# Performance work log

Measured on AMD Instinct MI355X. Metric: run time of the kernel, lower is better.

Reference implementation:

```python
import jax, jax.numpy as jnp
import numpy as np

B, S, L, U, E, V = 32, 64, 64, 512, 256, 32000

def setup_inputs() -> dict:
    key = jax.random.key(0)
    ks = jax.random.split(key, 12)
    sc = lambda *d: 0.02
    return {
        "target": jax.random.randint(ks[0], (B, S), 0, V),
        "encoder_outputs": jax.random.normal(ks[1], (B, L, U), jnp.float32),
        "enc_h0": jax.random.normal(ks[2], (B, U), jnp.float32),
        "enc_c0": jax.random.normal(ks[3], (B, U), jnp.float32),
        "emb": jax.random.normal(ks[4], (V, E), jnp.float32) * 0.02,
        "W_x": jax.random.normal(ks[5], (E, 4 * U), jnp.float32) * 0.02,
        "W_h": jax.random.normal(ks[6], (U, 4 * U), jnp.float32) * 0.02,
        "b_lstm": jnp.zeros((4 * U,), jnp.float32),
        "Wa": jax.random.normal(ks[7], (U, U), jnp.float32) * 0.02,
        "W_fc": jax.random.normal(ks[8], (2 * U, V), jnp.float32) * 0.02,
        "b_fc": jnp.zeros((V,), jnp.float32),
    }

def reference(target, encoder_outputs, enc_h0, enc_c0, emb, W_x, W_h, b_lstm, Wa, W_fc, b_fc):
    # Teacher forcing (teach_forcing_ran=1): input at step t is target[:, t-1],
    # producing outputs for t = 1 .. seq_maxlen-1.
    x_seq = emb[target[:, : S - 1]]                      # [B, S-1, E]
    x_seq = jnp.transpose(x_seq, (1, 0, 2))              # [S-1, B, E]
    enc_proj = jnp.einsum('blu,uv->blv', encoder_outputs, Wa)  # Luong 'general' projection

    def step(carry, x_t):
        h, c = carry
        z = x_t @ W_x + h @ W_h + b_lstm                 # [B, 4U]
        i, f, g, o = jnp.split(z, 4, axis=-1)            # keras gate order i,f,c,o
        i = jax.nn.sigmoid(i); f = jax.nn.sigmoid(f)
        g = jnp.tanh(g);       o = jax.nn.sigmoid(o)
        c = f * c + i * g
        h = o * jnp.tanh(c)
        score = jnp.einsum('bu,blu->bl', h, enc_proj)    # [B, L]
        attn = jax.nn.softmax(score, axis=-1)
        ctx = jnp.einsum('bl,blu->bu', attn, encoder_outputs)
        logits = jnp.tanh(jnp.concatenate([ctx, h], axis=-1) @ W_fc + b_fc)
        out_t = jax.nn.log_softmax(logits, axis=-1)      # [B, V]
        return (h, c), out_t

    (_, _), outs = jax.lax.scan(step, (enc_h0, enc_c0), x_seq)
    return jnp.transpose(outs, (1, 0, 2))                # [B, S-1, V]
```

## Files before the change

### kernel.cpp

```cpp
#include <hip/hip_runtime.h>
#include <stdint.h>

#define B_   32
#define T_   63
#define U_   512
#define E_   256
#define V_   32000
#define L_   64
#define FU_  2048
#define KFC_ 1024
#define MROW_ 2016

#define NFCX_ 250
#define NFCY_ 16
#define CCNT_BASE 1024

typedef float f32x4 __attribute__((ext_vector_type(4)));
typedef float f32x2 __attribute__((ext_vector_type(2)));
typedef __bf16 bf16x8 __attribute__((ext_vector_type(8)));

__device__ __forceinline__ unsigned short f2bf(float f) {
  union { float f; unsigned u; } v; v.f = f;
  unsigned u = v.u;
  u += 0x7FFFu + ((u >> 16) & 1u);
  return (unsigned short)(u >> 16);
}
__device__ __forceinline__ float bf2f(unsigned short h) {
  union { unsigned u; float f; } v; v.u = ((unsigned)h) << 16;
  return v.f;
}
__device__ __forceinline__ float fast_sigmoid(float x) {
  return 1.f / (1.f + __expf(-x));
}
__device__ __forceinline__ float fast_tanh(float x) {
  float e = __expf(2.f * x);
  return 1.f - 2.f / (e + 1.f);
}

__global__ __launch_bounds__(256) void k_prep(const int* __restrict__ target,
    const float* __restrict__ emb, const float* __restrict__ W_x,
    const float* __restrict__ b_lstm, const float* __restrict__ enc_out,
    const float* __restrict__ Wa, const float* __restrict__ W_h,
    const float* __restrict__ W_fc,
    unsigned short* __restrict__ fragWh, unsigned short* __restrict__ Zx,
    float* __restrict__ enc_proj, unsigned short* __restrict__ encT,
    unsigned short* __restrict__ WfcT,
    unsigned int* __restrict__ hcnt, float* __restrict__ row_sums) {
  __shared__ __align__(16) char smem[32768];
  const int bx = blockIdx.x;
  const int tid = threadIdx.x;

  if (bx < 512) {
    int idx = bx * 256 + tid;
    int lane = idx & 63;
    int kc   = (idx >> 6) & 15;
    int ct   = idx >> 10;
    int quad = lane >> 4, l15 = lane & 15;
    int col = ct * 16 + l15;
    unsigned short* dst = fragWh + (size_t)idx * 8;
#pragma unroll
    for (int j = 0; j < 8; ++j) {
      int k = kc * 32 + quad * 8 + j;
      dst[j] = f2bf(W_h[(size_t)k * FU_ + col]);
    }
  } else if (bx < 1016) {
    float* x_lds = (float*)smem;
    int r = bx - 512;
    int t = r % 63, cc = r / 63;
    for (int i = tid; i < B_ * E_; i += 256) {
      int b = i >> 8, e = i & 255;
      x_lds[i] = emb[(size_t)target[b * 64 + t] * E_ + e];
    }
    __syncthreads();
    int col = cc * 256 + tid;
    float acc[B_];
#pragma unroll
    for (int b = 0; b < B_; ++b) acc[b] = 0.f;
    for (int e4 = 0; e4 < E_ / 4; ++e4) {
      float w0 = W_x[(size_t)(4 * e4 + 0) * FU_ + col];
      float w1 = W_x[(size_t)(4 * e4 + 1) * FU_ + col];
      float w2 = W_x[(size_t)(4 * e4 + 2) * FU_ + col];
      float w3 = W_x[(size_t)(4 * e4 + 3) * FU_ + col];
#pragma unroll
      for (int b = 0; b < B_; ++b) {
        f32x4 xv = *(const f32x4*)&x_lds[b * E_ + 4 * e4];
        acc[b] += xv[0] * w0 + xv[1] * w1 + xv[2] * w2 + xv[3] * w3;
      }
    }
    float bias = b_lstm[col];
#pragma unroll
    for (int b = 0; b < B_; ++b)
      Zx[((size_t)(t * B_ + b)) * FU_ + col] = f2bf(acc[b] + bias);
  } else if (bx < 1272) {
    float* e_lds = (float*)smem;
    int r = bx - 1016;
    int rc = r & 127, cc = r >> 7;
    int row0 = rc * 16;
    for (int i = tid; i < 16 * U_; i += 256)
      e_lds[i] = enc_out[(size_t)(row0 + (i >> 9)) * U_ + (i & 511)];
    __syncthreads();
    int col = cc * 256 + tid;
    float acc[16];
#pragma unroll
    for (int q = 0; q < 16; ++q) acc[q] = 0.f;
    for (int k4 = 0; k4 < U_ / 4; ++k4) {
      float w0 = Wa[(size_t)(4 * k4 + 0) * U_ + col];
      float w1 = Wa[(size_t)(4 * k4 + 1) * U_ + col];
      float w2 = Wa[(size_t)(4 * k4 + 2) * U_ + col];
      float w3 = Wa[(size_t)(4 * k4 + 3) * U_ + col];
#pragma unroll
      for (int q = 0; q < 16; ++q) {
        f32x4 xv = *(const f32x4*)&e_lds[q * U_ + 4 * k4];
        acc[q] += xv[0] * w0 + xv[1] * w1 + xv[2] * w2 + xv[3] * w3;
      }
    }
#pragma unroll
    for (int q = 0; q < 16; ++q)
      enc_proj[(size_t)(row0 + q) * U_ + col] = acc[q];
  } else if (bx < 1528) {
    float (*tile)[65] = (float(*)[65])smem;
    int r = bx - 1272;
    int b = r & 31, uc = r >> 5;
#pragma unroll
    for (int i = 0; i < 16; ++i) {
      int idx = i * 256 + tid;
      int l = idx >> 6, u = idx & 63;
      tile[l][u] = enc_out[((size_t)b * L_ + l) * U_ + uc * 64 + u];
    }
    __syncthreads();
#pragma unroll
    for (int i = 0; i < 16; ++i) {
      int idx = i * 256 + tid;
      int u = idx >> 6, l = idx & 63;
      encT[((size_t)b * U_ + uc * 64 + u) * L_ + l] = f2bf(tile[l][u]);
    }
  } else if (bx < 1536) {
    int i = (bx - 1528) * 256 + tid;
    if (i < 2048) hcnt[i] = 0u;
    if (i < MROW_) row_sums[i] = 0.f;
  } else {
    float (*tile)[33] = (float(*)[33])smem;
    int r = bx - 1536;
    int nb = r % 1000, kb = r / 1000;
    int rr = tid >> 5, c = tid & 31;
#pragma unroll
    for (int i = 0; i < 4; ++i)
      tile[rr + 8 * i][c] = W_fc[(size_t)(kb * 32 + rr + 8 * i) * V_ + nb * 32 + c];
    __syncthreads();
#pragma unroll
    for (int i = 0; i < 4; ++i)
      WfcT[(size_t)(nb * 32 + rr + 8 * i) * KFC_ + kb * 32 + c] = f2bf(tile[c][rr + 8 * i]);
  }
}

__global__ __launch_bounds__(256, 1) void k_rec(const float* __restrict__ enc_h0,
    const float* __restrict__ enc_c0,
    const float* __restrict__ enc_proj, const unsigned short* __restrict__ Zx,
    const unsigned short* __restrict__ fragWh, const unsigned short* __restrict__ encT,
    unsigned int* hseq32,
    unsigned short* __restrict__ Afc,
    unsigned int* hcnt,
    const unsigned short* __restrict__ WfcT, const float* __restrict__ b_fc,
    float* __restrict__ out, float* __restrict__ row_sums) {
  __shared__ __align__(16) char smem[44160];

  const int tid = threadIdx.x;
  unsigned long long* hseq64 = (unsigned long long*)hseq32;

  if (blockIdx.x < 32) {
    unsigned short* h_lds = (unsigned short*)smem;
    float* z_lds = (float*)(smem + 33280);
    float* c_lds = (float*)(smem + 41984);

    const int g = blockIdx.x;
    const int w = tid >> 6;
    const int lane = tid & 63;
    const int quad = lane >> 4;
    const int l15 = lane & 15;
    const int b = tid >> 3;
    const int j = tid & 7;

    const unsigned short* bbase = fragWh + ((size_t)(w * 32 + g) * 16) * 64 * 8;
    bf16x8 bfr[16];
#pragma unroll
    for (int kc = 0; kc < 16; ++kc)
      bfr[kc] = *(const bf16x8*)(bbase + (size_t)(kc * 64 + lane) * 8);

    {
      int u = g * 16 + 2 * j;
      float h0a = enc_h0[(size_t)b * U_ + u];
      float h0b = enc_h0[(size_t)b * U_ + u + 1];
      unsigned pack = (unsigned)f2bf(h0a) | ((unsigned)f2bf(h0b) << 16);
      __hip_atomic_store(&hseq32[b * 256 + g * 8 + j], pack,
                         __ATOMIC_RELAXED, __HIP_MEMORY_SCOPE_AGENT);
      c_lds[b * 17 + 2 * j]     = enc_c0[(size_t)b * U_ + u];
      c_lds[b * 17 + 2 * j + 1] = enc_c0[(size_t)b * U_ + u + 1];
    }
    __syncthreads();
    if (tid == 0)
      __hip_atomic_fetch_add(&hcnt[0], 1u, __ATOMIC_RELAXED, __HIP_MEMORY_SCOPE_AGENT);

    for (int t = 0; t < T_; ++t) {
      const unsigned short* zxbase = Zx + ((size_t)(t * B_ + b)) * FU_ + g * 16 + 2 * j;
      unsigned zxp0 = *(const unsigned*)(zxbase + 0 * U_);
      unsigned zxp1 = *(const unsigned*)(zxbase + 1 * U_);
      unsigned zxp2 = *(const unsigned*)(zxbase + 2 * U_);
      unsigned zxp3 = *(const unsigned*)(zxbase + 3 * U_);

      if (tid == 0) {
        while (__hip_atomic_load(&hcnt[t * 16], __ATOMIC_RELAXED,
                                 __HIP_MEMORY_SCOPE_AGENT) < 32u)
          __builtin_amdgcn_s_sleep(1);
      }
      __syncthreads();

      const unsigned long long* hp = hseq64 + (size_t)t * (B_ * U_ / 4);
#pragma unroll
      for (int i = 0; i < 16; ++i) {
        int idx = i * 256 + tid;
        int hb = idx >> 7, u0 = (idx & 127) * 4;
        unsigned long long v = __hip_atomic_load(&hp[idx], __ATOMIC_RELAXED,
                                                 __HIP_MEMORY_SCOPE_AGENT);
        *(unsigned long long*)&h_lds[hb * 520 + u0] = v;
      }
      __syncthreads();

      f32x4 acc0 = {0.f, 0.f, 0.f, 0.f}, acc1 = {0.f, 0.f, 0.f, 0.f};
#pragma unroll
      for (int kc = 0; kc < 16; ++kc) {
        bf16x8 a0 = *(const bf16x8*)&h_lds[l15 * 520 + kc * 32 + quad * 8];
        bf16x8 a1 = *(const bf16x8*)&h_lds[(16 + l15) * 520 + kc * 32 + quad * 8];
        acc0 = __builtin_amdgcn_mfma_f32_16x16x32_bf16(a0, bfr[kc], acc0, 0, 0, 0);
        acc1 = __builtin_amdgcn_mfma_f32_16x16x32_bf16(a1, bfr[kc], acc1, 0, 0, 0);
      }
#pragma unroll
      for (int r = 0; r < 4; ++r) {
        z_lds[(quad * 4 + r) * 68 + w * 16 + l15] = acc0[r];
        z_lds[(16 + quad * 4 + r) * 68 + w * 16 + l15] = acc1[r];
      }
      __syncthreads();

      {
        int up0 = 2 * j, up1 = 2 * j + 1;
        float zi0 = z_lds[b * 68 + 0 + up0] + bf2f((unsigned short)(zxp0 & 0xFFFFu));
        float zi1 = z_lds[b * 68 + 0 + up1] + bf2f((unsigned short)(zxp0 >> 16));
        float zf0 = z_lds[b * 68 + 16 + up0] + bf2f((unsigned short)(zxp1 & 0xFFFFu));
        float zf1 = z_lds[b * 68 + 16 + up1] + bf2f((unsigned short)(zxp1 >> 16));
        float zg0 = z_lds[b * 68 + 32 + up0] + bf2f((unsigned short)(zxp2 & 0xFFFFu));
        float zg1 = z_lds[b * 68 + 32 + up1] + bf2f((unsigned short)(zxp2 >> 16));
        float zo0 = z_lds[b * 68 + 48 + up0] + bf2f((unsigned short)(zxp3 & 0xFFFFu));
        float zo1 = z_lds[b * 68 + 48 + up1] + bf2f((unsigned short)(zxp3 >> 16));
        float i0 = fast_sigmoid(zi0), i1 = fast_sigmoid(zi1);
        float f0 = fast_sigmoid(zf0), f1 = fast_sigmoid(zf1);
        float g0 = fast_tanh(zg0),    g1 = fast_tanh(zg1);
        float o0 = fast_sigmoid(zo0), o1 = fast_sigmoid(zo1);
        float c0 = f0 * c_lds[b * 17 + up0] + i0 * g0;
        float c1 = f1 * c_lds[b * 17 + up1] + i1 * g1;
        c_lds[b * 17 + up0] = c0;
        c_lds[b * 17 + up1] = c1;
        float h0 = o0 * fast_tanh(c0);
        float h1 = o1 * fast_tanh(c1);
        unsigned pack = (unsigned)f2bf(h0) | ((unsigned)f2bf(h1) << 16);
        __hip_atomic_store(&hseq32[(size_t)(t + 1) * (B_ * U_ / 2) + b * 256 + g * 8 + j],
                           pack, __ATOMIC_RELAXED, __HIP_MEMORY_SCOPE_AGENT);
        __hip_atomic_store(
            (unsigned*)&Afc[(size_t)(t * B_ + b) * KFC_ + U_ + g * 16 + 2 * j],
            pack, __ATOMIC_RELAXED, __HIP_MEMORY_SCOPE_AGENT);
      }
      __syncthreads();
      if (tid == 0)
        __hip_atomic_fetch_add(&hcnt[(t + 1) * 16], 1u,
                               __ATOMIC_RELAXED, __HIP_MEMORY_SCOPE_AGENT);
    }
  } else if (blockIdx.x < 64) {
    float* h_sh    = (float*)smem;
    float* sc_part = (float*)(smem + 2048);
    float* probs   = (float*)(smem + 3072);

    const int b = blockIdx.x - 32;
    for (int t = 0; t < T_; ++t) {
      if (tid == 0) {
        while (__hip_atomic_load(&hcnt[(t + 1) * 16], __ATOMIC_RELAXED,
                                 __HIP_MEMORY_SCOPE_AGENT) < 32u)
          __builtin_amdgcn_s_sleep(2);
      }
      __syncthreads();
      if (tid < 128) {
        unsigned long long v = __hip_atomic_load(
            &hseq64[(size_t)(t + 1) * (B_ * U_ / 4) + b * 128 + tid],
            __ATOMIC_RELAXED, __HIP_MEMORY_SCOPE_AGENT);
        int u0 = tid * 4;
        h_sh[u0 + 0] = bf2f((unsigned short)(v & 0xFFFFu));
        h_sh[u0 + 1] = bf2f((unsigned short)((v >> 16) & 0xFFFFu));
        h_sh[u0 + 2] = bf2f((unsigned short)((v >> 32) & 0xFFFFu));
        h_sh[u0 + 3] = bf2f((unsigned short)((v >> 48) & 0xFFFFu));
      }
      __syncthreads();
      {
        int l = tid & 63, part = tid >> 6;
        const float* ep = enc_proj + ((size_t)(b * L_ + l)) * U_ + part * 128;
        const float* hs = h_sh + part * 128;
        float s = 0.f;
#pragma unroll 8
        for (int u = 0; u < 128; u += 4) {
          f32x4 e = *(const f32x4*)(ep + u);
          s += hs[u] * e[0] + hs[u + 1] * e[1] + hs[u + 2] * e[2] + hs[u + 3] * e[3];
        }
        sc_part[part * L_ + l] = s;
      }
      __syncthreads();
      if (tid < 64) {
        float s = sc_part[tid] + sc_part[64 + tid] + sc_part[128 + tid] + sc_part[192 + tid];
        float m = s;
#pragma unroll
        for (int off = 32; off >= 1; off >>= 1) m = fmaxf(m, __shfl_xor(m, off));
        float e = __expf(s - m);
        float sum = e;
#pragma unroll
        for (int off = 32; off >= 1; off >>= 1) sum += __shfl_xor(sum, off);
        probs[tid] = e / sum;
      }
      __syncthreads();
      {
        int u0 = 2 * tid;
        const unsigned short* ep0 = encT + ((size_t)b * U_ + u0) * L_;
        float c0 = 0.f, c1 = 0.f;
#pragma unroll
        for (int l8 = 0; l8 < 8; ++l8) {
          bf16x8 e0 = *(const bf16x8*)(ep0 + l8 * 8);
          bf16x8 e1 = *(const bf16x8*)(ep0 + L_ + l8 * 8);
#pragma unroll
          for (int q = 0; q < 8; ++q) {
            float p = probs[l8 * 8 + q];
            c0 += p * (float)e0[q];
            c1 += p * (float)e1[q];
          }
        }
        unsigned pack = (unsigned)f2bf(c0) | ((unsigned)f2bf(c1) << 16);
        __hip_atomic_store((unsigned*)&Afc[(size_t)(t * B_ + b) * KFC_ + u0], pack,
                           __ATOMIC_RELAXED, __HIP_MEMORY_SCOPE_AGENT);
      }
      __syncthreads();
      if (tid == 0)
        __hip_atomic_fetch_add(&hcnt[CCNT_BASE + t * 16], 1u,
                               __ATOMIC_RELAXED, __HIP_MEMORY_SCOPE_AGENT);
    }
  } else {
    unsigned short* At = (unsigned short*)smem;
    unsigned short* Bt = (unsigned short*)(smem + 8192);
    float* rs = (float*)(smem + 16384);

    const int idx = blockIdx.x - 64;
    const int cx = idx % NFCX_, ry = idx / NFCX_;
    int t_hi = 4 * ry + 3; if (t_hi > T_ - 1) t_hi = T_ - 1;

    if (tid == 0) {
      while (__hip_atomic_load(&hcnt[CCNT_BASE + t_hi * 16], __ATOMIC_RELAXED,
                               __HIP_MEMORY_SCOPE_AGENT) < 32u)
        __builtin_amdgcn_s_sleep(32);
    }
    __syncthreads();

    const int w = tid >> 6, lane = tid & 63, quad = lane >> 4, l15 = lane & 15;
    const int row0 = ry * 128, col0 = cx * 128;
    const int mh = (w >> 1) * 64, nh = (w & 1) * 64;

    f32x4 acc[4][4];
#pragma unroll
    for (int i = 0; i < 4; ++i)
#pragma unroll
      for (int j = 0; j < 4; ++j) { f32x4 z = {0.f, 0.f, 0.f, 0.f}; acc[i][j] = z; }

    for (int kt = 0; kt < KFC_ / 32; ++kt) {
      int k0 = kt * 32;
#pragma unroll
      for (int i = 0; i < 2; ++i) {
        int lin = i * 256 + tid;
        int r = lin >> 2, s = lin & 3;
        int gseg = (s - (r >> 1)) & 3;
        f32x4 va = *(const f32x4*)(Afc + ((size_t)(row0 + r)) * KFC_ + k0 + gseg * 8);
        *(f32x4*)&At[r * 32 + s * 8] = va;
        f32x4 vb = *(const f32x4*)(WfcT + ((size_t)(col0 + r)) * KFC_ + k0 + gseg * 8);
        *(f32x4*)&Bt[r * 32 + s * 8] = vb;
      }
      __syncthreads();
      bf16x8 a[4], b[4];
#pragma unroll
      for (int i = 0; i < 4; ++i) {
        int m = mh + i * 16 + l15;
        a[i] = *(const bf16x8*)&At[m * 32 + (((quad + (m >> 1)) & 3) * 8)];
        int n = nh + i * 16 + l15;
        b[i] = *(const bf16x8*)&Bt[n * 32 + (((quad + (n >> 1)) & 3) * 8)];
      }
#pragma unroll
      for (int i = 0; i < 4; ++i)
#pragma unroll
        for (int j = 0; j < 4; ++j)
          acc[i][j] = __builtin_amdgcn_mfma_f32_16x16x32_bf16(a[i], b[j], acc[i][j], 0, 0, 0);
      __syncthreads();
    }

    if (tid < 128) rs[tid] = 0.f;
    __syncthreads();
    float bv[4];
#pragma unroll
    for (int j = 0; j < 4; ++j) bv[j] = b_fc[col0 + nh + j * 16 + l15];
    float rp[4][4];
#pragma unroll
    for (int i = 0; i < 4; ++i)
#pragma unroll
      for (int r = 0; r < 4; ++r) rp[i][r] = 0.f;
#pragma unroll
    for (int i = 0; i < 4; ++i) {
#pragma unroll
      for (int j = 0; j < 4; ++j) {
        int cg = col0 + nh + j * 16 + l15;
#pragma unroll
        for (int r = 0; r < 4; ++r) {
          float val = fast_tanh(acc[i][j][r] + bv[j]);
          int rg = row0 + mh + i * 16 + quad * 4 + r;
          if (rg < MROW_) {
            int b = rg & 31, t = rg >> 5;
            out[((size_t)(b * T_ + t)) * V_ + cg] = val;
          }
          rp[i][r] += __expf(val);
        }
      }
    }
#pragma unroll
    for (int i = 0; i < 4; ++i)
#pragma unroll
      for (int r = 0; r < 4; ++r) {
        float v = rp[i][r];
        v += __shfl_xor(v, 1); v += __shfl_xor(v, 2);
        v += __shfl_xor(v, 4); v += __shfl_xor(v, 8);
        if (l15 == 0) atomicAdd(&rs[mh + i * 16 + quad * 4 + r], v);
      }
    __syncthreads();
    if (tid < 128) {
      int rg = row0 + tid;
      if (rg < MROW_) atomicAdd(&row_sums[rg], rs[tid]);
    }
  }
}

__global__ __launch_bounds__(256) void k_lsm(float* __restrict__ out,
                                             const float* __restrict__ row_sums, int n4) {
  int i = blockIdx.x * 256 + threadIdx.x;
  if (i >= n4) return;
  f32x4* o4 = (f32x4*)out;
  f32x4 v = o4[i];
  int r = i / 8000;
  int b = r / 63, t = r - b * 63;
  float ls = __logf(row_sums[t * 32 + b]);
  v[0] -= ls; v[1] -= ls; v[2] -= ls; v[3] -= ls;
  o4[i] = v;
}

extern "C" void kernel_launch(void* const* d_in, const int* in_sizes, int n_in,
                              void* d_out, int out_size, void* d_ws, size_t ws_size,
                              hipStream_t stream) {
  const int*   target  = (const int*)d_in[0];
  const float* enc_out = (const float*)d_in[1];
  const float* enc_h0  = (const float*)d_in[2];
  const float* enc_c0  = (const float*)d_in[3];
  const float* emb     = (const float*)d_in[4];
  const float* W_x     = (const float*)d_in[5];
  const float* W_h     = (const float*)d_in[6];
  const float* b_lstm  = (const float*)d_in[7];
  const float* Wa      = (const float*)d_in[8];
  const float* W_fc    = (const float*)d_in[9];
  const float* b_fc    = (const float*)d_in[10];
  float* out = (float*)d_out;
  char* ws = (char*)d_ws;

  unsigned int*   hcnt     = (unsigned int*)(ws + 0);
  float*          row_sums = (float*)(ws + 8192);
  unsigned short* fragWh   = (unsigned short*)(ws + 16384);
  unsigned int*   hseq32   = (unsigned int*)(ws + 2113536);
  unsigned short* Zx       = (unsigned short*)(ws + 4210688);
  float*          enc_proj = (float*)(ws + 12468224);
  unsigned short* Afc      = (unsigned short*)(ws + 16662528);
  unsigned short* encT     = (unsigned short*)(ws + 20856832);
  unsigned short* WfcT     = (unsigned short*)(ws + 22953984);

  k_prep <<<dim3(33536),        dim3(256), 0, stream>>>(target, emb, W_x, b_lstm,
                                                        enc_out, Wa, W_h, W_fc,
                                                        fragWh, Zx, enc_proj, encT,
                                                        WfcT, hcnt, row_sums);
  k_rec  <<<dim3(64 + NFCX_ * NFCY_), dim3(256), 0, stream>>>(enc_h0, enc_c0,
                                                        enc_proj, Zx, fragWh, encT,
                                                        hseq32, Afc, hcnt,
                                                        WfcT, b_fc, out, row_sums);
  k_lsm  <<<dim3(63000),        dim3(256), 0, stream>>>(out, row_sums, 16128000);
}
```

Baseline: 1.146 ms.

## Fuse W_fc transpose and log-softmax into persistent recurrent kernel

Moves the W_fc bf16 transpose out of the prep kernel into the first row of FC blocks in the persistent kernel. Other FC blocks wait on per-column flags before using those weights. The separate log-softmax kernel is removed: each FC row group counts completed blocks and then subtracts the log-sum from its output rows in place. It also raises wave priority for the recurrent blocks and batches the h loads before the LDS stores. This removes two launches and overlaps the weight conversion with the recurrence, but adds spin-waits and relaxed-atomic cross-block dependencies.

```diff
diff --git a/kernel.cpp b/kernel.cpp
--- a/kernel.cpp
+++ b/kernel.cpp
@@ -14,6 +14,7 @@
 #define NFCX_ 250
 #define NFCY_ 16
 #define CCNT_BASE 1024
+#define AFC_FLAG_U32 (2016 * 512)
 
 typedef float f32x4 __attribute__((ext_vector_type(4)));
 typedef float f32x2 __attribute__((ext_vector_type(2)));
@@ -41,11 +42,10 @@
     const float* __restrict__ emb, const float* __restrict__ W_x,
     const float* __restrict__ b_lstm, const float* __restrict__ enc_out,
     const float* __restrict__ Wa, const float* __restrict__ W_h,
-    const float* __restrict__ W_fc,
     unsigned short* __restrict__ fragWh, unsigned short* __restrict__ Zx,
     float* __restrict__ enc_proj, unsigned short* __restrict__ encT,
-    unsigned short* __restrict__ WfcT,
-    unsigned int* __restrict__ hcnt, float* __restrict__ row_sums) {
+    unsigned int* __restrict__ hcnt, float* __restrict__ row_sums,
+    unsigned int* __restrict__ AfcFlags) {
   __shared__ __align__(16) char smem[32768];
   const int bx = blockIdx.x;
   const int tid = threadIdx.x;
@@ -134,22 +134,14 @@
       int u = idx >> 6, l = idx & 63;
       encT[((size_t)b * U_ + uc * 64 + u) * L_ + l] = f2bf(tile[l][u]);
     }
-  } else if (bx < 1536) {
+  } else {
     int i = (bx - 1528) * 256 + tid;
-    if (i < 2048) hcnt[i] = 0u;
+    hcnt[i] = 0u;
     if (i < MROW_) row_sums[i] = 0.f;
-  } else {
-    float (*tile)[33] = (float(*)[33])smem;
-    int r = bx - 1536;
-    int nb = r % 1000, kb = r / 1000;
-    int rr = tid >> 5, c = tid & 31;
-#pragma unroll
-    for (int i = 0; i < 4; ++i)
-      tile[rr + 8 * i][c] = W_fc[(size_t)(kb * 32 + rr + 8 * i) * V_ + nb * 32 + c];
-    __syncthreads();
-#pragma unroll
-    for (int i = 0; i < 4; ++i)
-      WfcT[(size_t)(nb * 32 + rr + 8 * i) * KFC_ + kb * 32 + c] = f2bf(tile[c][rr + 8 * i]);
+    AfcFlags[i * 4 + 0] = 0u;
+    AfcFlags[i * 4 + 1] = 0u;
+    AfcFlags[i * 4 + 2] = 0u;
+    AfcFlags[i * 4 + 3] = 0u;
   }
 }
 
@@ -160,12 +152,14 @@
     unsigned int* hseq32,
     unsigned short* __restrict__ Afc,
     unsigned int* hcnt,
-    const unsigned short* __restrict__ WfcT, const float* __restrict__ b_fc,
-    float* __restrict__ out, float* __restrict__ row_sums) {
+    unsigned short* __restrict__ WfcT, const float* __restrict__ b_fc,
+    float* __restrict__ out, float* __restrict__ row_sums,
+    const float* __restrict__ W_fc) {
   __shared__ __align__(16) char smem[44160];
 
   const int tid = threadIdx.x;
   unsigned long long* hseq64 = (unsigned long long*)hseq32;
+  unsigned int* AfcFlags = (unsigned int*)Afc + AFC_FLAG_U32;
 
   if (blockIdx.x < 32) {
     unsigned short* h_lds = (unsigned short*)smem;
@@ -185,6 +179,8 @@
 #pragma unroll
     for (int kc = 0; kc < 16; ++kc)
       bfr[kc] = *(const bf16x8*)(bbase + (size_t)(kc * 64 + lane) * 8);
+
+    __builtin_amdgcn_s_setprio(1);
 
     {
       int u = g * 16 + 2 * j;
@@ -215,13 +211,17 @@
       __syncthreads();
 
       const unsigned long long* hp = hseq64 + (size_t)t * (B_ * U_ / 4);
+      unsigned long long hv[16];
+#pragma unroll
+      for (int i = 0; i < 16; ++i) {
+        hv[i] = __hip_atomic_load(&hp[i * 256 + tid], __ATOMIC_RELAXED,
+                                  __HIP_MEMORY_SCOPE_AGENT);
+      }
 #pragma unroll
       for (int i = 0; i < 16; ++i) {
         int idx = i * 256 + tid;
         int hb = idx >> 7, u0 = (idx & 127) * 4;
-        unsigned long long v = __hip_atomic_load(&hp[idx], __ATOMIC_RELAXED,
-                                                 __HIP_MEMORY_SCOPE_AGENT);
-        *(unsigned long long*)&h_lds[hb * 520 + u0] = v;
+        *(unsigned long long*)&h_lds[hb * 520 + u0] = hv[i];
       }
       __syncthreads();
 
@@ -277,6 +277,7 @@
     float* sc_part = (float*)(smem + 2048);
     float* probs   = (float*)(smem + 3072);
 
+    __builtin_amdgcn_s_setprio(1);
     const int b = blockIdx.x - 32;
     for (int t = 0; t < T_; ++t) {
       if (tid == 0) {
@@ -349,12 +350,53 @@
     unsigned short* At = (unsigned short*)smem;
     unsigned short* Bt = (unsigned short*)(smem + 8192);
     float* rs = (float*)(smem + 16384);
+    float* lsb = (float*)(smem + 16896);
 
     const int idx = blockIdx.x - 64;
     const int cx = idx % NFCX_, ry = idx / NFCX_;
     int t_hi = 4 * ry + 3; if (t_hi > T_ - 1) t_hi = T_ - 1;
 
+    if (ry == 0) {
+      float* tile = (float*)smem;
+      const int n0 = cx * 128;
+      for (int kt2 = 0; kt2 < 32; ++kt2) {
+        int k0 = kt2 * 32;
+#pragma unroll
+        for (int it = 0; it < 4; ++it) {
+          int lin = it * 256 + tid;
+          int k = lin >> 5, nq = lin & 31;
+          f32x4 v = *(const f32x4*)(W_fc + (size_t)(k0 + k) * V_ + n0 + nq * 4);
+          *(f32x4*)&tile[k * 132 + nq * 4] = v;
+        }
+        __syncthreads();
+#pragma unroll
+        for (int it = 0; it < 4; ++it) {
+          int lin = it * 256 + tid;
+          int n = lin >> 3, kq = lin & 7;
+          float a0 = tile[(kq * 4 + 0) * 132 + n];
+          float a1 = tile[(kq * 4 + 1) * 132 + n];
+          float a2 = tile[(kq * 4 + 2) * 132 + n];
+          float a3 = tile[(kq * 4 + 3) * 132 + n];
+          unsigned long long pk =
+              (unsigned long long)((unsigned)f2bf(a0) | ((unsigned)f2bf(a1) << 16)) |
+              ((unsigned long long)((unsigned)f2bf(a2) | ((unsigned)f2bf(a3) << 16)) << 32);
+          __hip_atomic_store(
+              (unsigned long long*)&WfcT[(size_t)(n0 + n) * KFC_ + k0 + kq * 4], pk,
+              __ATOMIC_RELAXED, __HIP_MEMORY_SCOPE_AGENT);
+        }
+        __syncthreads();
+      }
+      if (tid == 0)
+        __hip_atomic_store(&AfcFlags[cx * 16], 1u,
+                           __ATOMIC_RELAXED, __HIP_MEMORY_SCOPE_AGENT);
+    }
+
     if (tid == 0) {
+      if (ry != 0) {
+        while (__hip_atomic_load(&AfcFlags[cx * 16], __ATOMIC_RELAXED,
+                                 __HIP_MEMORY_SCOPE_AGENT) == 0u)
+          __builtin_amdgcn_s_sleep(16);
+      }
       while (__hip_atomic_load(&hcnt[CCNT_BASE + t_hi * 16], __ATOMIC_RELAXED,
                                __HIP_MEMORY_SCOPE_AGENT) < 32u)
         __builtin_amdgcn_s_sleep(32);
@@ -421,7 +463,10 @@
           int rg = row0 + mh + i * 16 + quad * 4 + r;
           if (rg < MROW_) {
             int b = rg & 31, t = rg >> 5;
-            out[((size_t)(b * T_ + t)) * V_ + cg] = val;
+            union { float f; unsigned u; } cv; cv.f = val;
+            __hip_atomic_store(
+                (unsigned*)&out[((size_t)(b * T_ + t)) * V_ + cg], cv.u,
+                __ATOMIC_RELAXED, __HIP_MEMORY_SCOPE_AGENT);
           }
           rp[i][r] += __expf(val);
         }
@@ -441,20 +486,35 @@
       int rg = row0 + tid;
       if (rg < MROW_) atomicAdd(&row_sums[rg], rs[tid]);
     }
+    __syncthreads();
+    if (tid == 0)
+      __hip_atomic_fetch_add(&AfcFlags[4096 + ry * 16], 1u,
+                             __ATOMIC_RELAXED, __HIP_MEMORY_SCOPE_AGENT);
+
+    {
+      int rg = ry * 128 + cx;
+      if (cx < 128 && rg < MROW_) {
+        if (tid == 0) {
+          while (__hip_atomic_load(&AfcFlags[4096 + ry * 16], __ATOMIC_RELAXED,
+                                   __HIP_MEMORY_SCOPE_AGENT) < (unsigned)NFCX_)
+            __builtin_amdgcn_s_sleep(16);
+          union { unsigned u; float f; } cv;
+          cv.u = __hip_atomic_load((unsigned*)&row_sums[rg], __ATOMIC_RELAXED,
+                                   __HIP_MEMORY_SCOPE_AGENT);
+          lsb[0] = __logf(cv.f);
+        }
+        __syncthreads();
+        float ls = lsb[0];
+        int b = rg & 31, t = rg >> 5;
+        float* orow = out + (size_t)(b * T_ + t) * V_;
+        for (int c = tid * 4; c < V_; c += 1024) {
+          f32x4 v = *(const f32x4*)(orow + c);
+          v[0] -= ls; v[1] -= ls; v[2] -= ls; v[3] -= ls;
+          *(f32x4*)(orow + c) = v;
+        }
+      }
+    }
   }
-}
-
-__global__ __launch_bounds__(256) void k_lsm(float* __restrict__ out,
-                                             const float* __restrict__ row_sums, int n4) {
-  int i = blockIdx.x * 256 + threadIdx.x;
-  if (i >= n4) return;
-  f32x4* o4 = (f32x4*)out;
-  f32x4 v = o4[i];
-  int r = i / 8000;
-  int b = r / 63, t = r - b * 63;
-  float ls = __logf(row_sums[t * 32 + b]);
-  v[0] -= ls; v[1] -= ls; v[2] -= ls; v[3] -= ls;
-  o4[i] = v;
 }
 
 extern "C" void kernel_launch(void* const* d_in, const int* in_sizes, int n_in,
@@ -484,13 +544,15 @@
   unsigned short* encT     = (unsigned short*)(ws + 20856832);
   unsigned short* WfcT     = (unsigned short*)(ws + 22953984);
 
-  k_prep <<<dim3(33536),        dim3(256), 0, stream>>>(target, emb, W_x, b_lstm,
-                                                        enc_out, Wa, W_h, W_fc,
+  unsigned int* AfcFlags = (unsigned int*)(ws + 16662528 + (size_t)AFC_FLAG_U32 * 4);
+
+  k_prep <<<dim3(1536),         dim3(256), 0, stream>>>(target, emb, W_x, b_lstm,
+                                                        enc_out, Wa, W_h,
                                                         fragWh, Zx, enc_proj, encT,
-                                                        WfcT, hcnt, row_sums);
+                                                        hcnt, row_sums, AfcFlags);
   k_rec  <<<dim3(64 + NFCX_ * NFCY_), dim3(256), 0, stream>>>(enc_h0, enc_c0,
                                                         enc_proj, Zx, fragWh, encT,
                                                         hseq32, Afc, hcnt,
-                                                        WfcT, b_fc, out, row_sums);
-  k_lsm  <<<dim3(63000),        dim3(256), 0, stream>>>(out, row_sums, 16128000);
-}
+                                                        WfcT, b_fc, out, row_sums,
+                                                        W_fc);
+}
```

Result: slower. 1.317 ms (+14.9%).
